# Optimization experiments

Measured on AMD Instinct MI355X. Metric: run time of the kernel, lower is better.

## Reference

```python
import jax, jax.numpy as jnp
import numpy as np

B = 16384
WIDE_DIM = 256          # 32 wide features * dim 8
DEEP_DIM = 1024         # 64 deep features * embedding_dim 16
SHARED = [2048, 1024, 512]
DOMAIN = [512, 256]
NUM_DOMAINS = 8


def setup_inputs() -> dict:
    key = jax.random.key(0)
    ks = jax.random.split(key, 20)
    s = 0.01  # embedding_init_var-style small init
    inp = {
        "wide_features": jax.random.normal(ks[0], (B, WIDE_DIM), jnp.float32),
        "deep_features": jax.random.normal(ks[1], (B, DEEP_DIM), jnp.float32),
        "domain_ids": jax.random.randint(ks[2], (B,), 0, NUM_DOMAINS, jnp.int64),
        # shared MLP (weights stored [in, out])
        "W1": jax.random.normal(ks[3], (DEEP_DIM, SHARED[0]), jnp.float32) * s,
        "b1": jnp.zeros((SHARED[0],), jnp.float32),
        "W2": jax.random.normal(ks[4], (SHARED[0], SHARED[1]), jnp.float32) * s,
        "b2": jnp.zeros((SHARED[1],), jnp.float32),
        "W3": jax.random.normal(ks[5], (SHARED[1], SHARED[2]), jnp.float32) * s,
        "b3": jnp.zeros((SHARED[2],), jnp.float32),
        # domain-specific MLP
        "Wd1": jax.random.normal(ks[6], (SHARED[2], DOMAIN[0]), jnp.float32) * s,
        "bd1": jnp.zeros((DOMAIN[0],), jnp.float32),
        "Wd2": jax.random.normal(ks[7], (DOMAIN[0], DOMAIN[1]), jnp.float32) * s,
        "bd2": jnp.zeros((DOMAIN[1],), jnp.float32),
        # per-domain output heads: Linear(DOMAIN[-1], 1) per domain
        "Wh": jax.random.normal(ks[8], (NUM_DOMAINS, DOMAIN[1]), jnp.float32) * s,
        "bh": jnp.zeros((NUM_DOMAINS,), jnp.float32),
    }
    return inp


def reference(wide_features, deep_features, domain_ids,
              W1, b1, W2, b2, W3, b3, Wd1, bd1, Wd2, bd2, Wh, bh):
    # wide part: sum embedding output to a scalar logit per sample [B, 1]
    wide = jnp.sum(wide_features, axis=1, keepdims=True)
    # shared deep MLP
    h = jax.nn.relu(deep_features @ W1 + b1)
    h = jax.nn.relu(h @ W2 + b2)
    shared = jax.nn.relu(h @ W3 + b3)          # [B, 512]
    # domain-specific tower (shared across domains)
    d = jax.nn.relu(shared @ Wd1 + bd1)
    d = jax.nn.relu(d @ Wd2 + bd2)             # [B, 256]
    # per-sample domain head routing: gather head weights, fused dot
    w = Wh[domain_ids]                          # [B, 256]
    head = jnp.sum(d * w, axis=1, keepdims=True) + bh[domain_ids][:, None]  # [B, 1]
    out = jax.nn.sigmoid(wide + head)
    return (out, shared, d)
```

## Files before the change

### kernel.cpp

```cpp
#include <hip/hip_runtime.h>
#include <hip/hip_bf16.h>


typedef __attribute__((ext_vector_type(8))) short short8;
typedef __attribute__((ext_vector_type(4))) float f32x4;

static __device__ __forceinline__ unsigned short f2bf_bits(float x) {
  __hip_bfloat16 h = __float2bfloat16(x);
  return __builtin_bit_cast(unsigned short, h);
}
static __device__ __forceinline__ float bf_bits2f(unsigned short u) {
  __hip_bfloat16 h = __builtin_bit_cast(__hip_bfloat16, u);
  return __bfloat162float(h);
}

static __device__ __forceinline__ void gload16(const void* g, void* l) {
  __builtin_amdgcn_global_load_lds(
      (const __attribute__((address_space(1))) void*)g,
      (__attribute__((address_space(3))) void*)l, 16, 0, 0);
}

static __device__ __forceinline__ unsigned lds_u32(const void* p) {
  return (unsigned)(uintptr_t)(const __attribute__((address_space(3))) void*)p;
}

static __device__ __forceinline__ short8 dsr(unsigned addr) {
  short8 r;
  asm volatile("ds_read_b128 %0, %1" : "=v"(r) : "v"(addr));
  return r;
}

#define MFMA16(a, b, c) __builtin_amdgcn_mfma_f32_16x16x32_bf16((a), (b), (c), 0, 0, 0)

__global__ void transpose_convert(const float* __restrict__ W,
                                  __hip_bfloat16* __restrict__ Wt,
                                  int K, int N) {
  __shared__ float tile[64][65];
  const int k0 = blockIdx.y * 64;
  const int n0 = blockIdx.x * 64;
  const int t  = threadIdx.x;
  const int tn = t & 63;
  const int t4 = t >> 6;
#pragma unroll
  for (int p = 0; p < 16; ++p) {
    int kl = p * 4 + t4;
    tile[kl][tn] = W[(size_t)(k0 + kl) * N + (n0 + tn)];
  }
  __syncthreads();
#pragma unroll
  for (int p = 0; p < 16; ++p) {
    int nl = p * 4 + t4;
    Wt[(size_t)(n0 + nl) * K + (k0 + tn)] = __float2bfloat16(tile[tn][nl]);
  }
}

__global__ void f32_to_bf16(const float* __restrict__ in,
                            unsigned short* __restrict__ out, int n8) {
  int i = blockIdx.x * blockDim.x + threadIdx.x;
  if (i >= n8) return;
  const f32x4* p = (const f32x4*)in + (size_t)i * 2;
  f32x4 a = p[0], b = p[1];
  short8 o;
  o[0] = (short)f2bf_bits(a[0]); o[1] = (short)f2bf_bits(a[1]);
  o[2] = (short)f2bf_bits(a[2]); o[3] = (short)f2bf_bits(a[3]);
  o[4] = (short)f2bf_bits(b[0]); o[5] = (short)f2bf_bits(b[1]);
  o[6] = (short)f2bf_bits(b[2]); o[7] = (short)f2bf_bits(b[3]);
  *(short8*)(out + (size_t)i * 8) = o;
}

__global__ __launch_bounds__(512, 2) void gemm_8p(
    const __hip_bfloat16* __restrict__ A,
    const __hip_bfloat16* __restrict__ Bt,
    const float* __restrict__ bias,
    __hip_bfloat16* __restrict__ Cb,
    float* __restrict__ Cf,
    int N, int K, int nbx) {
  __shared__ char lds[131072];

  const int tid  = threadIdx.x;
  const int lane = tid & 63;
  const int wid  = tid >> 6;
  const int wm   = wid >> 2;
  const int wn   = wid & 3;

  const int nwg = gridDim.x;
  const int cpx = nwg >> 3;
  const int id  = blockIdx.x;
  const int swz = (id & 7) * cpx + (id >> 3);
  const int bm  = (swz / nbx) * 256;
  const int bn  = (swz % nbx) * 256;

  const int ln15 = lane & 15;
  const unsigned cswz = (unsigned)((((lane >> 4) ^ (lane & 7)) << 4));

  const unsigned lbase = lds_u32(lds);
  const unsigned arow0 = lbase + (unsigned)(wm * 128 + ln15) * 128u + cswz;
  const unsigned brow0 = lbase + 32768u + (unsigned)(wn * 64 + ln15) * 128u + cswz;

  const int nt = K >> 6;

  const int swc = (tid & 7) ^ ((tid >> 3) & 7);
  const __hip_bfloat16* baseA = A  + (size_t)(bm + (tid >> 3)) * K + swc * 8;
  const __hip_bfloat16* baseB = Bt + (size_t)(bn + (tid >> 3)) * K + swc * 8;
  const unsigned ldst0 = (unsigned)(wid * 1024);

  auto stage = [&](int kt, int half, int isB) {
    const __hip_bfloat16* base = isB ? baseB : baseA;
    char* dst = lds + ((kt & 1) * 65536) + (isB ? 32768 : 0) + half * 16384;
#pragma unroll
    for (int q = 0; q < 2; ++q) {
      gload16(base + (size_t)((half * 128 + q * 64) * K + kt * 64),
              dst + q * 8192 + ldst0);
    }
  };

  f32x4 acc[8][4] = {};

  stage(0, 0, 1); stage(0, 0, 0); stage(0, 1, 1); stage(0, 1, 0);
  if (nt > 1) { stage(1, 0, 1); stage(1, 0, 0); }

  for (int t = 0; t < nt; ++t) {
    const unsigned po = (unsigned)(t & 1) * 65536u;
    short8 a_[4][2], b0_[2][2], b1_[2][2];

    if (t + 1 < nt) asm volatile("s_waitcnt vmcnt(4)");
    else            asm volatile("s_waitcnt vmcnt(0)");
    __builtin_amdgcn_s_barrier();
#pragma unroll
    for (int mi = 0; mi < 4; ++mi) a_[mi][0] = dsr(arow0 + po + (unsigned)(mi * 2048));
#pragma unroll
    for (int nj = 0; nj < 2; ++nj) b0_[nj][0] = dsr(brow0 + po + (unsigned)(nj * 2048));
#pragma unroll
    for (int mi = 0; mi < 4; ++mi) a_[mi][1] = dsr((arow0 + po + (unsigned)(mi * 2048)) ^ 64u);
#pragma unroll
    for (int nj = 0; nj < 2; ++nj) b0_[nj][1] = dsr((brow0 + po + (unsigned)(nj * 2048)) ^ 64u);
    if (t + 1 < nt) stage(t + 1, 1, 1);
    asm volatile("s_waitcnt lgkmcnt(6)");
    __builtin_amdgcn_sched_barrier(0);
    __builtin_amdgcn_s_setprio(1);
#pragma unroll
    for (int mi = 0; mi < 4; ++mi)
#pragma unroll
      for (int nj = 0; nj < 2; ++nj)
        acc[mi][nj] = MFMA16(a_[mi][0], b0_[nj][0], acc[mi][nj]);
    asm volatile("s_waitcnt lgkmcnt(0)");
    __builtin_amdgcn_sched_barrier(0);
#pragma unroll
    for (int mi = 0; mi < 4; ++mi)
#pragma unroll
      for (int nj = 0; nj < 2; ++nj)
        acc[mi][nj] = MFMA16(a_[mi][1], b0_[nj][1], acc[mi][nj]);
    __builtin_amdgcn_s_setprio(0);

#pragma unroll
    for (int nj = 0; nj < 2; ++nj) {
      unsigned bd = brow0 + po + (unsigned)((nj + 2) * 2048);
      b1_[nj][0] = dsr(bd); b1_[nj][1] = dsr(bd ^ 64u);
    }
    if (t + 1 < nt) stage(t + 1, 1, 0);
    __builtin_amdgcn_s_barrier();
    asm volatile("s_waitcnt lgkmcnt(0)");
    __builtin_amdgcn_sched_barrier(0);
    __builtin_amdgcn_s_setprio(1);
#pragma unroll
    for (int kk = 0; kk < 2; ++kk)
#pragma unroll
      for (int mi = 0; mi < 4; ++mi)
#pragma unroll
        for (int nj = 0; nj < 2; ++nj)
          acc[mi][nj + 2] = MFMA16(a_[mi][kk], b1_[nj][kk], acc[mi][nj + 2]);
    __builtin_amdgcn_s_setprio(0);

#pragma unroll
    for (int mi = 0; mi < 4; ++mi) {
      unsigned ad = arow0 + po + (unsigned)((mi + 4) * 2048);
      a_[mi][0] = dsr(ad); a_[mi][1] = dsr(ad ^ 64u);
    }
    __builtin_amdgcn_s_barrier();
    if (t + 2 < nt) stage(t + 2, 0, 1);
    asm volatile("s_waitcnt lgkmcnt(0)");
    __builtin_amdgcn_sched_barrier(0);
    __builtin_amdgcn_s_setprio(1);
#pragma unroll
    for (int kk = 0; kk < 2; ++kk)
#pragma unroll
      for (int mi = 0; mi < 4; ++mi)
#pragma unroll
        for (int nj = 0; nj < 2; ++nj)
          acc[mi + 4][nj] = MFMA16(a_[mi][kk], b0_[nj][kk], acc[mi + 4][nj]);
    __builtin_amdgcn_s_setprio(0);

    __builtin_amdgcn_s_barrier();
    if (t + 2 < nt) stage(t + 2, 0, 0);
    __builtin_amdgcn_s_setprio(1);
#pragma unroll
    for (int kk = 0; kk < 2; ++kk)
#pragma unroll
      for (int mi = 0; mi < 4; ++mi)
#pragma unroll
        for (int nj = 0; nj < 2; ++nj)
          acc[mi + 4][nj + 2] = MFMA16(a_[mi][kk], b1_[nj][kk], acc[mi + 4][nj + 2]);
    __builtin_amdgcn_s_setprio(0);
  }

  float biasv[4];
#pragma unroll
  for (int nj = 0; nj < 4; ++nj)
    biasv[nj] = bias[bn + wn * 64 + nj * 16 + ln15];

#pragma unroll
  for (int mi = 0; mi < 8; ++mi) {
    int row0 = bm + wm * 128 + mi * 16 + (lane >> 4) * 4;
#pragma unroll
    for (int nj = 0; nj < 4; ++nj) {
      int col = bn + wn * 64 + nj * 16 + ln15;
#pragma unroll
      for (int r = 0; r < 4; ++r) {
        float v = acc[mi][nj][r] + biasv[nj];
        v = v > 0.f ? v : 0.f;
        size_t idx = (size_t)(row0 + r) * N + col;
        Cb[idx] = __float2bfloat16(v);
        if (Cf) Cf[idx] = v;
      }
    }
  }
}

__global__ __launch_bounds__(256, 2) void gemm_bt(
    const __hip_bfloat16* __restrict__ A,
    const __hip_bfloat16* __restrict__ Bt,
    const float* __restrict__ bias,
    __hip_bfloat16* __restrict__ Cb,
    float* __restrict__ Cf,
    int N, int K) {
  __shared__ char lds[32768];

  const int tid  = threadIdx.x;
  const int lane = tid & 63;
  const int wid  = tid >> 6;
  const int wm   = wid >> 1;
  const int wn   = wid & 1;
  const int bm   = blockIdx.y * 128;
  const int bn   = blockIdx.x * 128;

  f32x4 acc[4][4] = {};

  const int srow = tid >> 3;
  const int sk   = (tid & 7) * 8;
  const int kTiles = K >> 6;

  for (int kt = 0; kt < kTiles; ++kt) {
    __syncthreads();
    const __hip_bfloat16* ga = A  + (size_t)(bm + srow) * K + kt * 64 + sk;
    const __hip_bfloat16* gb = Bt + (size_t)(bn + srow) * K + kt * 64 + sk;
#pragma unroll
    for (int p = 0; p < 4; ++p) {
      gload16(ga + (size_t)(p * 32) * K, &lds[p * 4096 + wid * 1024]);
      gload16(gb + (size_t)(p * 32) * K, &lds[16384 + p * 4096 + wid * 1024]);
    }
    __syncthreads();

#pragma unroll
    for (int kk = 0; kk < 2; ++kk) {
      short8 avec[4], bvec[4];
#pragma unroll
      for (int i = 0; i < 4; ++i) {
        int row = wm * 64 + i * 16 + (lane & 15);
        avec[i] = *(const short8*)&lds[row * 128 + kk * 64 + (lane >> 4) * 16];
      }
#pragma unroll
      for (int j = 0; j < 4; ++j) {
        int row = wn * 64 + j * 16 + (lane & 15);
        bvec[j] = *(const short8*)&lds[16384 + row * 128 + kk * 64 + (lane >> 4) * 16];
      }
#pragma unroll
      for (int i = 0; i < 4; ++i)
#pragma unroll
        for (int j = 0; j < 4; ++j)
          acc[i][j] = MFMA16(avec[i], bvec[j], acc[i][j]);
    }
  }

  float biasv[4];
#pragma unroll
  for (int j = 0; j < 4; ++j)
    biasv[j] = bias[bn + wn * 64 + j * 16 + (lane & 15)];

#pragma unroll
  for (int i = 0; i < 4; ++i) {
    int row0 = bm + wm * 64 + i * 16 + (lane >> 4) * 4;
#pragma unroll
    for (int j = 0; j < 4; ++j) {
      int col = bn + wn * 64 + j * 16 + (lane & 15);
#pragma unroll
      for (int r = 0; r < 4; ++r) {
        float v = acc[i][j][r] + biasv[j];
        v = v > 0.f ? v : 0.f;
        size_t idx = (size_t)(row0 + r) * N + col;
        Cb[idx] = __float2bfloat16(v);
        if (Cf) Cf[idx] = v;
      }
    }
  }
}

__global__ __launch_bounds__(256) void head_kernel(
    const float* __restrict__ wide,
    const __hip_bfloat16* __restrict__ D,
    const int* __restrict__ dom,
    const float* __restrict__ Wh,
    const float* __restrict__ bh,
    float* __restrict__ out, int B) {
  const int wid  = threadIdx.x >> 6;
  const int lane = threadIdx.x & 63;
  const int row  = blockIdx.x * 4 + wid;
  if (row >= B) return;
  const int dm = dom[row];

  f32x4 wv = ((const f32x4*)(wide + (size_t)row * 256))[lane];
  float tot = wv[0] + wv[1] + wv[2] + wv[3];

  const unsigned short* drow = (const unsigned short*)(D + (size_t)row * 256);
  ushort4 dv = ((const ushort4*)drow)[lane];
  f32x4 hv = ((const f32x4*)(Wh + (size_t)dm * 256))[lane];
  tot += bf_bits2f(dv.x) * hv[0] + bf_bits2f(dv.y) * hv[1] +
         bf_bits2f(dv.z) * hv[2] + bf_bits2f(dv.w) * hv[3];

#pragma unroll
  for (int off = 32; off > 0; off >>= 1) tot += __shfl_xor(tot, off);

  if (lane == 0) {
    float x = tot + bh[dm];
    out[row] = 1.f / (1.f + __expf(-x));
  }
}

extern "C" void kernel_launch(void* const* d_in, const int* in_sizes, int n_in,
                              void* d_out, int out_size, void* d_ws, size_t ws_size,
                              hipStream_t stream) {
  const float* wide = (const float*)d_in[0];
  const float* deep = (const float*)d_in[1];
  const int*   dom  = (const int*)d_in[2];
  const float* W1  = (const float*)d_in[3];
  const float* b1  = (const float*)d_in[4];
  const float* W2  = (const float*)d_in[5];
  const float* b2  = (const float*)d_in[6];
  const float* W3  = (const float*)d_in[7];
  const float* b3  = (const float*)d_in[8];
  const float* Wd1 = (const float*)d_in[9];
  const float* bd1 = (const float*)d_in[10];
  const float* Wd2 = (const float*)d_in[11];
  const float* bd2 = (const float*)d_in[12];
  const float* Wh  = (const float*)d_in[13];
  const float* bh  = (const float*)d_in[14];
  float* out = (float*)d_out;

  const int B = 16384;
  char* ws = (char*)d_ws;
  __hip_bfloat16* buf0 = (__hip_bfloat16*)ws;
  __hip_bfloat16* buf1 = (__hip_bfloat16*)(ws + 33554432ull);
  __hip_bfloat16* W1t  = (__hip_bfloat16*)(ws + 100663296ull);
  __hip_bfloat16* W2t  = W1t + 2048 * 1024;
  __hip_bfloat16* W3t  = W2t + 1024 * 2048;
  __hip_bfloat16* Wd1t = W3t + 512 * 1024;
  __hip_bfloat16* Wd2t = Wd1t + 512 * 512;

  transpose_convert<<<dim3(2048 / 64, 1024 / 64), 256, 0, stream>>>(W1, W1t, 1024, 2048);
  transpose_convert<<<dim3(1024 / 64, 2048 / 64), 256, 0, stream>>>(W2, W2t, 2048, 1024);
  transpose_convert<<<dim3(512 / 64, 1024 / 64), 256, 0, stream>>>(W3, W3t, 1024, 512);
  transpose_convert<<<dim3(512 / 64, 512 / 64), 256, 0, stream>>>(Wd1, Wd1t, 512, 512);
  transpose_convert<<<dim3(256 / 64, 512 / 64), 256, 0, stream>>>(Wd2, Wd2t, 512, 256);

  {
    int n8 = B * 1024 / 8;
    f32_to_bf16<<<(n8 + 255) / 256, 256, 0, stream>>>(deep, (unsigned short*)buf0, n8);
  }

  float* shared_out = out + B;
  float* d_out_f    = out + B + (size_t)B * 512;

  gemm_8p<<<dim3((2048 / 256) * (B / 256)), 512, 0, stream>>>(
      buf0, W1t, b1, buf1, nullptr, 2048, 1024, 2048 / 256);
  gemm_8p<<<dim3((1024 / 256) * (B / 256)), 512, 0, stream>>>(
      buf1, W2t, b2, buf0, nullptr, 1024, 2048, 1024 / 256);
  gemm_bt<<<dim3(512 / 128, B / 128), 256, 0, stream>>>(buf0, W3t, b3, buf1, shared_out, 512, 1024);
  gemm_bt<<<dim3(512 / 128, B / 128), 256, 0, stream>>>(buf1, Wd1t, bd1, buf0, nullptr, 512, 512);
  gemm_bt<<<dim3(256 / 128, B / 128), 256, 0, stream>>>(buf0, Wd2t, bd2, buf1, d_out_f, 256, 512);

  head_kernel<<<B / 4, 256, 0, stream>>>(wide, buf1, dom, Wh, bh, out, B);
}
```

Measured before the change: 234.2 us.

## Add reordered-pipeline GEMM for layer 2 and 128x256-tile GEMM for layers 3-4

Adds gemm_8pq, a variant of the 256x256 8-wave GEMM for the W2 layer. It loads all B fragments up front and prefetches the next tile's low A fragments across the loop boundary, so LDS reads overlap MFMA work better. Adds gemm_128, a 512-thread kernel with 128x256 tiles, and uses it for the W3 and Wd1 layers in place of the 256-thread 128x128 gemm_bt. The intent is better reuse and scheduling for the mid-size GEMMs, at the cost of more register pressure and more complex waitcnt and barrier logic that could be miscounted.

```diff
diff --git a/kernel.cpp b/kernel.cpp
--- a/kernel.cpp
+++ b/kernel.cpp
@@ -31,6 +31,9 @@
 }
 
 #define MFMA16(a, b, c) __builtin_amdgcn_mfma_f32_16x16x32_bf16((a), (b), (c), 0, 0, 0)
+#define SB0() __builtin_amdgcn_sched_barrier(0)
+#define PRIO(x) __builtin_amdgcn_s_setprio(x)
+#define BAR() __builtin_amdgcn_s_barrier()
 
 __global__ void transpose_convert(const float* __restrict__ W,
                                   __hip_bfloat16* __restrict__ Wt,
@@ -125,7 +128,7 @@
 
     if (t + 1 < nt) asm volatile("s_waitcnt vmcnt(4)");
     else            asm volatile("s_waitcnt vmcnt(0)");
-    __builtin_amdgcn_s_barrier();
+    BAR();
 #pragma unroll
     for (int mi = 0; mi < 4; ++mi) a_[mi][0] = dsr(arow0 + po + (unsigned)(mi * 2048));
 #pragma unroll
@@ -136,21 +139,21 @@
     for (int nj = 0; nj < 2; ++nj) b0_[nj][1] = dsr((brow0 + po + (unsigned)(nj * 2048)) ^ 64u);
     if (t + 1 < nt) stage(t + 1, 1, 1);
     asm volatile("s_waitcnt lgkmcnt(6)");
-    __builtin_amdgcn_sched_barrier(0);
-    __builtin_amdgcn_s_setprio(1);
+    SB0();
+    PRIO(1);
 #pragma unroll
     for (int mi = 0; mi < 4; ++mi)
 #pragma unroll
       for (int nj = 0; nj < 2; ++nj)
         acc[mi][nj] = MFMA16(a_[mi][0], b0_[nj][0], acc[mi][nj]);
     asm volatile("s_waitcnt lgkmcnt(0)");
-    __builtin_amdgcn_sched_barrier(0);
+    SB0();
 #pragma unroll
     for (int mi = 0; mi < 4; ++mi)
 #pragma unroll
       for (int nj = 0; nj < 2; ++nj)
         acc[mi][nj] = MFMA16(a_[mi][1], b0_[nj][1], acc[mi][nj]);
-    __builtin_amdgcn_s_setprio(0);
+    PRIO(0);
 
 #pragma unroll
     for (int nj = 0; nj < 2; ++nj) {
@@ -158,10 +161,10 @@
       b1_[nj][0] = dsr(bd); b1_[nj][1] = dsr(bd ^ 64u);
     }
     if (t + 1 < nt) stage(t + 1, 1, 0);
-    __builtin_amdgcn_s_barrier();
-    asm volatile("s_waitcnt lgkmcnt(0)");
-    __builtin_amdgcn_sched_barrier(0);
-    __builtin_amdgcn_s_setprio(1);
+    BAR();
+    asm volatile("s_waitcnt lgkmcnt(0)");
+    SB0();
+    PRIO(1);
 #pragma unroll
     for (int kk = 0; kk < 2; ++kk)
 #pragma unroll
@@ -169,18 +172,18 @@
 #pragma unroll
         for (int nj = 0; nj < 2; ++nj)
           acc[mi][nj + 2] = MFMA16(a_[mi][kk], b1_[nj][kk], acc[mi][nj + 2]);
-    __builtin_amdgcn_s_setprio(0);
+    PRIO(0);
 
 #pragma unroll
     for (int mi = 0; mi < 4; ++mi) {
       unsigned ad = arow0 + po + (unsigned)((mi + 4) * 2048);
       a_[mi][0] = dsr(ad); a_[mi][1] = dsr(ad ^ 64u);
     }
-    __builtin_amdgcn_s_barrier();
+    BAR();
     if (t + 2 < nt) stage(t + 2, 0, 1);
     asm volatile("s_waitcnt lgkmcnt(0)");
-    __builtin_amdgcn_sched_barrier(0);
-    __builtin_amdgcn_s_setprio(1);
+    SB0();
+    PRIO(1);
 #pragma unroll
     for (int kk = 0; kk < 2; ++kk)
 #pragma unroll
@@ -188,11 +191,11 @@
 #pragma unroll
         for (int nj = 0; nj < 2; ++nj)
           acc[mi + 4][nj] = MFMA16(a_[mi][kk], b0_[nj][kk], acc[mi + 4][nj]);
-    __builtin_amdgcn_s_setprio(0);
-
-    __builtin_amdgcn_s_barrier();
+    PRIO(0);
+
+    BAR();
     if (t + 2 < nt) stage(t + 2, 0, 0);
-    __builtin_amdgcn_s_setprio(1);
+    PRIO(1);
 #pragma unroll
     for (int kk = 0; kk < 2; ++kk)
 #pragma unroll
@@ -200,7 +203,7 @@
 #pragma unroll
         for (int nj = 0; nj < 2; ++nj)
           acc[mi + 4][nj + 2] = MFMA16(a_[mi][kk], b1_[nj][kk], acc[mi + 4][nj + 2]);
-    __builtin_amdgcn_s_setprio(0);
+    PRIO(0);
   }
 
   float biasv[4];
@@ -211,6 +214,341 @@
 #pragma unroll
   for (int mi = 0; mi < 8; ++mi) {
     int row0 = bm + wm * 128 + mi * 16 + (lane >> 4) * 4;
+#pragma unroll
+    for (int nj = 0; nj < 4; ++nj) {
+      int col = bn + wn * 64 + nj * 16 + ln15;
+#pragma unroll
+      for (int r = 0; r < 4; ++r) {
+        float v = acc[mi][nj][r] + biasv[nj];
+        v = v > 0.f ? v : 0.f;
+        size_t idx = (size_t)(row0 + r) * N + col;
+        Cb[idx] = __float2bfloat16(v);
+        if (Cf) Cf[idx] = v;
+      }
+    }
+  }
+}
+
+__global__ __launch_bounds__(512, 2) void gemm_8pq(
+    const __hip_bfloat16* __restrict__ A,
+    const __hip_bfloat16* __restrict__ Bt,
+    const float* __restrict__ bias,
+    __hip_bfloat16* __restrict__ Cb,
+    int N, int K, int nbx) {
+  __shared__ char lds[131072];
+
+  const int tid  = threadIdx.x;
+  const int lane = tid & 63;
+  const int wid  = tid >> 6;
+  const int wm   = wid >> 2;
+  const int wn   = wid & 3;
+
+  const int nwg = gridDim.x;
+  const int cpx = nwg >> 3;
+  const int id  = blockIdx.x;
+  const int swz = (id & 7) * cpx + (id >> 3);
+  const int bm  = (swz / nbx) * 256;
+  const int bn  = (swz % nbx) * 256;
+
+  const int ln15 = lane & 15;
+  const unsigned cswz = (unsigned)((((lane >> 4) ^ (lane & 7)) << 4));
+
+  const unsigned lbase = lds_u32(lds);
+  const unsigned arow0 = lbase + (unsigned)(wm * 128 + ln15) * 128u + cswz;
+  const unsigned brow0 = lbase + 32768u + (unsigned)(wn * 64 + ln15) * 128u + cswz;
+
+  const int nt = K >> 6;
+
+  const int swc = (tid & 7) ^ ((tid >> 3) & 7);
+  const __hip_bfloat16* baseA = A  + (size_t)(bm + (tid >> 3)) * K + swc * 8;
+  const __hip_bfloat16* baseB = Bt + (size_t)(bn + (tid >> 3)) * K + swc * 8;
+  const unsigned ldst0 = (unsigned)(wid * 1024);
+
+  auto stage = [&](int kt, int half, int isB) {
+    const __hip_bfloat16* base = isB ? baseB : baseA;
+    char* dst = lds + ((kt & 1) * 65536) + (isB ? 32768 : 0) + half * 16384;
+#pragma unroll
+    for (int q = 0; q < 2; ++q) {
+      gload16(base + (size_t)((half * 128 + q * 64) * K + kt * 64),
+              dst + q * 8192 + ldst0);
+    }
+  };
+
+  f32x4 acc[8][4] = {};
+  short8 aLo[4][2], aHi[4][2], b0v[2][2], b1v[2][2];
+
+  stage(0, 0, 1); stage(0, 0, 0); stage(0, 1, 1); stage(0, 1, 0);
+  if (nt > 1) {
+    stage(1, 0, 1); stage(1, 0, 0);
+    asm volatile("s_waitcnt vmcnt(4)");
+  } else {
+    asm volatile("s_waitcnt vmcnt(0)");
+  }
+  BAR();
+#pragma unroll
+  for (int mi = 0; mi < 4; ++mi) {
+    unsigned ad = arow0 + (unsigned)(mi * 2048);
+    aLo[mi][0] = dsr(ad); aLo[mi][1] = dsr(ad ^ 64u);
+  }
+
+  for (int t = 0; t < nt; ++t) {
+    const unsigned po = (unsigned)(t & 1) * 65536u;
+    const unsigned pn = po ^ 65536u;
+
+    asm volatile("s_waitcnt lgkmcnt(0)");
+    SB0();
+#pragma unroll
+    for (int nj = 0; nj < 2; ++nj) b0v[nj][0] = dsr(brow0 + po + (unsigned)(nj * 2048));
+#pragma unroll
+    for (int nj = 0; nj < 2; ++nj) b0v[nj][1] = dsr((brow0 + po + (unsigned)(nj * 2048)) ^ 64u);
+#pragma unroll
+    for (int nj = 0; nj < 2; ++nj) b1v[nj][0] = dsr(brow0 + po + (unsigned)((nj + 2) * 2048));
+#pragma unroll
+    for (int nj = 0; nj < 2; ++nj) b1v[nj][1] = dsr((brow0 + po + (unsigned)((nj + 2) * 2048)) ^ 64u);
+    asm volatile("s_waitcnt lgkmcnt(6)");
+    SB0();
+    PRIO(1);
+#pragma unroll
+    for (int mi = 0; mi < 4; ++mi)
+#pragma unroll
+      for (int nj = 0; nj < 2; ++nj)
+        acc[mi][nj] = MFMA16(aLo[mi][0], b0v[nj][0], acc[mi][nj]);
+    asm volatile("s_waitcnt lgkmcnt(4)");
+    SB0();
+#pragma unroll
+    for (int mi = 0; mi < 4; ++mi)
+#pragma unroll
+      for (int nj = 0; nj < 2; ++nj)
+        acc[mi][nj] = MFMA16(aLo[mi][1], b0v[nj][1], acc[mi][nj]);
+    PRIO(0);
+    if (t + 1 < nt) stage(t + 1, 1, 1);
+    BAR();
+
+    asm volatile("s_waitcnt lgkmcnt(0)");
+    SB0();
+#pragma unroll
+    for (int mi = 0; mi < 4; ++mi) {
+      unsigned ad = arow0 + po + (unsigned)((mi + 4) * 2048);
+      aHi[mi][0] = dsr(ad); aHi[mi][1] = dsr(ad ^ 64u);
+    }
+    PRIO(1);
+#pragma unroll
+    for (int kk = 0; kk < 2; ++kk)
+#pragma unroll
+      for (int mi = 0; mi < 4; ++mi)
+#pragma unroll
+        for (int nj = 0; nj < 2; ++nj)
+          acc[mi][nj + 2] = MFMA16(aLo[mi][kk], b1v[nj][kk], acc[mi][nj + 2]);
+    PRIO(0);
+    if (t + 1 < nt) stage(t + 1, 1, 0);
+    BAR();
+
+    asm volatile("s_waitcnt lgkmcnt(0)");
+    SB0();
+    PRIO(1);
+#pragma unroll
+    for (int kk = 0; kk < 2; ++kk)
+#pragma unroll
+      for (int mi = 0; mi < 4; ++mi)
+#pragma unroll
+        for (int nj = 0; nj < 2; ++nj)
+          acc[mi + 4][nj] = MFMA16(aHi[mi][kk], b0v[nj][kk], acc[mi + 4][nj]);
+    PRIO(0);
+    if (t + 2 < nt) stage(t + 2, 0, 1);
+    if (t + 1 < nt) {
+      if (t + 2 < nt) asm volatile("s_waitcnt vmcnt(2)");
+      else            asm volatile("s_waitcnt vmcnt(0)");
+    }
+    BAR();
+
+    SB0();
+    if (t + 1 < nt) {
+#pragma unroll
+      for (int mi = 0; mi < 4; ++mi) {
+        unsigned ad = arow0 + pn + (unsigned)(mi * 2048);
+        aLo[mi][0] = dsr(ad); aLo[mi][1] = dsr(ad ^ 64u);
+      }
+    }
+    PRIO(1);
+#pragma unroll
+    for (int kk = 0; kk < 2; ++kk)
+#pragma unroll
+      for (int mi = 0; mi < 4; ++mi)
+#pragma unroll
+        for (int nj = 0; nj < 2; ++nj)
+          acc[mi + 4][nj + 2] = MFMA16(aHi[mi][kk], b1v[nj][kk], acc[mi + 4][nj + 2]);
+    PRIO(0);
+    if (t + 2 < nt) stage(t + 2, 0, 0);
+    BAR();
+  }
+
+  float biasv[4];
+#pragma unroll
+  for (int nj = 0; nj < 4; ++nj)
+    biasv[nj] = bias[bn + wn * 64 + nj * 16 + ln15];
+
+#pragma unroll
+  for (int mi = 0; mi < 8; ++mi) {
+    int row0 = bm + wm * 128 + mi * 16 + (lane >> 4) * 4;
+#pragma unroll
+    for (int nj = 0; nj < 4; ++nj) {
+      int col = bn + wn * 64 + nj * 16 + ln15;
+#pragma unroll
+      for (int r = 0; r < 4; ++r) {
+        float v = acc[mi][nj][r] + biasv[nj];
+        v = v > 0.f ? v : 0.f;
+        Cb[(size_t)(row0 + r) * N + col] = __float2bfloat16(v);
+      }
+    }
+  }
+}
+
+__global__ __launch_bounds__(512, 2) void gemm_128(
+    const __hip_bfloat16* __restrict__ A,
+    const __hip_bfloat16* __restrict__ Bt,
+    const float* __restrict__ bias,
+    __hip_bfloat16* __restrict__ Cb,
+    float* __restrict__ Cf,
+    int N, int K, int nbx) {
+  __shared__ char lds[98304];
+
+  const int tid  = threadIdx.x;
+  const int lane = tid & 63;
+  const int wid  = tid >> 6;
+  const int wm   = wid >> 2;
+  const int wn   = wid & 3;
+
+  const int nwg = gridDim.x;
+  const int cpx = nwg >> 3;
+  const int id  = blockIdx.x;
+  const int swz = (id & 7) * cpx + (id >> 3);
+  const int bm  = (swz / nbx) * 128;
+  const int bn  = (swz % nbx) * 256;
+
+  const int ln15 = lane & 15;
+  const unsigned cswz = (unsigned)((((lane >> 4) ^ (lane & 7)) << 4));
+
+  const unsigned lbase = lds_u32(lds);
+  const unsigned arow0 = lbase + (unsigned)(wm * 64 + ln15) * 128u + cswz;
+  const unsigned brow0 = lbase + 16384u + (unsigned)(wn * 64 + ln15) * 128u + cswz;
+
+  const int nt = K >> 6;
+
+  const int swc = (tid & 7) ^ ((tid >> 3) & 7);
+  const __hip_bfloat16* baseA = A  + (size_t)(bm + (tid >> 3)) * K + swc * 8;
+  const __hip_bfloat16* baseB = Bt + (size_t)(bn + (tid >> 3)) * K + swc * 8;
+  const unsigned ldst0 = (unsigned)(tid * 16);
+
+  auto stageA = [&](int kt, int half) {
+    char* dst = lds + ((kt & 1) * 49152) + half * 8192;
+    gload16(baseA + (size_t)((half * 64) * K + kt * 64), dst + ldst0);
+  };
+  auto stageB = [&](int kt, int half) {
+    char* dst = lds + ((kt & 1) * 49152) + 16384 + half * 16384;
+#pragma unroll
+    for (int q = 0; q < 2; ++q) {
+      gload16(baseB + (size_t)((half * 128 + q * 64) * K + kt * 64),
+              dst + q * 8192 + ldst0);
+    }
+  };
+
+  f32x4 acc[4][4] = {};
+
+  stageB(0, 0); stageA(0, 0); stageB(0, 1); stageA(0, 1);
+  if (nt > 1) { stageB(1, 0); stageA(1, 0); }
+
+  for (int t = 0; t < nt; ++t) {
+    const unsigned po = (unsigned)(t & 1) * 49152u;
+    short8 a_[4][2], b_[4][2];
+
+    if (t + 1 < nt) asm volatile("s_waitcnt vmcnt(3)");
+    else            asm volatile("s_waitcnt vmcnt(0)");
+    BAR();
+#pragma unroll
+    for (int mi = 0; mi < 2; ++mi) a_[mi][0] = dsr(arow0 + po + (unsigned)(mi * 2048));
+#pragma unroll
+    for (int nj = 0; nj < 2; ++nj) b_[nj][0] = dsr(brow0 + po + (unsigned)(nj * 2048));
+#pragma unroll
+    for (int mi = 0; mi < 2; ++mi) a_[mi][1] = dsr((arow0 + po + (unsigned)(mi * 2048)) ^ 64u);
+#pragma unroll
+    for (int nj = 0; nj < 2; ++nj) b_[nj][1] = dsr((brow0 + po + (unsigned)(nj * 2048)) ^ 64u);
+    if (t + 1 < nt) stageB(t + 1, 1);
+    asm volatile("s_waitcnt lgkmcnt(4)");
+    SB0();
+    PRIO(1);
+#pragma unroll
+    for (int mi = 0; mi < 2; ++mi)
+#pragma unroll
+      for (int nj = 0; nj < 2; ++nj)
+        acc[mi][nj] = MFMA16(a_[mi][0], b_[nj][0], acc[mi][nj]);
+    asm volatile("s_waitcnt lgkmcnt(0)");
+    SB0();
+#pragma unroll
+    for (int mi = 0; mi < 2; ++mi)
+#pragma unroll
+      for (int nj = 0; nj < 2; ++nj)
+        acc[mi][nj] = MFMA16(a_[mi][1], b_[nj][1], acc[mi][nj]);
+    PRIO(0);
+
+#pragma unroll
+    for (int nj = 0; nj < 2; ++nj) {
+      unsigned bd = brow0 + po + (unsigned)((nj + 2) * 2048);
+      b_[nj + 2][0] = dsr(bd); b_[nj + 2][1] = dsr(bd ^ 64u);
+    }
+    if (t + 1 < nt) stageA(t + 1, 1);
+    BAR();
+    asm volatile("s_waitcnt lgkmcnt(0)");
+    SB0();
+    PRIO(1);
+#pragma unroll
+    for (int kk = 0; kk < 2; ++kk)
+#pragma unroll
+      for (int mi = 0; mi < 2; ++mi)
+#pragma unroll
+        for (int nj = 0; nj < 2; ++nj)
+          acc[mi][nj + 2] = MFMA16(a_[mi][kk], b_[nj + 2][kk], acc[mi][nj + 2]);
+    PRIO(0);
+
+#pragma unroll
+    for (int mi = 0; mi < 2; ++mi) {
+      unsigned ad = arow0 + po + (unsigned)((mi + 2) * 2048);
+      a_[mi + 2][0] = dsr(ad); a_[mi + 2][1] = dsr(ad ^ 64u);
+    }
+    BAR();
+    if (t + 2 < nt) stageB(t + 2, 0);
+    asm volatile("s_waitcnt lgkmcnt(0)");
+    SB0();
+    PRIO(1);
+#pragma unroll
+    for (int kk = 0; kk < 2; ++kk)
+#pragma unroll
+      for (int mi = 0; mi < 2; ++mi)
+#pragma unroll
+        for (int nj = 0; nj < 2; ++nj)
+          acc[mi + 2][nj] = MFMA16(a_[mi + 2][kk], b_[nj][kk], acc[mi + 2][nj]);
+    PRIO(0);
+
+    BAR();
+    if (t + 2 < nt) stageA(t + 2, 0);
+    PRIO(1);
+#pragma unroll
+    for (int kk = 0; kk < 2; ++kk)
+#pragma unroll
+      for (int mi = 0; mi < 2; ++mi)
+#pragma unroll
+        for (int nj = 0; nj < 2; ++nj)
+          acc[mi + 2][nj + 2] = MFMA16(a_[mi + 2][kk], b_[nj + 2][kk], acc[mi + 2][nj + 2]);
+    PRIO(0);
+  }
+
+  float biasv[4];
+#pragma unroll
+  for (int nj = 0; nj < 4; ++nj)
+    biasv[nj] = bias[bn + wn * 64 + nj * 16 + ln15];
+
+#pragma unroll
+  for (int mi = 0; mi < 4; ++mi) {
+    int row0 = bm + wm * 64 + mi * 16 + (lane >> 4) * 4;
 #pragma unroll
     for (int nj = 0; nj < 4; ++nj) {
       int col = bn + wn * 64 + nj * 16 + ln15;
@@ -381,10 +719,12 @@
 
   gemm_8p<<<dim3((2048 / 256) * (B / 256)), 512, 0, stream>>>(
       buf0, W1t, b1, buf1, nullptr, 2048, 1024, 2048 / 256);
-  gemm_8p<<<dim3((1024 / 256) * (B / 256)), 512, 0, stream>>>(
-      buf1, W2t, b2, buf0, nullptr, 1024, 2048, 1024 / 256);
-  gemm_bt<<<dim3(512 / 128, B / 128), 256, 0, stream>>>(buf0, W3t, b3, buf1, shared_out, 512, 1024);
-  gemm_bt<<<dim3(512 / 128, B / 128), 256, 0, stream>>>(buf1, Wd1t, bd1, buf0, nullptr, 512, 512);
+  gemm_8pq<<<dim3((1024 / 256) * (B / 256)), 512, 0, stream>>>(
+      buf1, W2t, b2, buf0, 1024, 2048, 1024 / 256);
+  gemm_128<<<dim3((B / 128) * (512 / 256)), 512, 0, stream>>>(
+      buf0, W3t, b3, buf1, shared_out, 512, 1024, 512 / 256);
+  gemm_128<<<dim3((B / 128) * (512 / 256)), 512, 0, stream>>>(
+      buf1, Wd1t, bd1, buf0, nullptr, 512, 512, 512 / 256);
   gemm_bt<<<dim3(256 / 128, B / 128), 256, 0, stream>>>(buf0, Wd2t, bd2, buf1, d_out_f, 256, 512);
 
   head_kernel<<<B / 4, 256, 0, stream>>>(wide, buf1, dom, Wh, bh, out, B);
```

Result: faster. 227.3 us (-2.9%).
